# Optimization experiments

Hardware: AMD Instinct MI355X
Metric: run time of the kernel (lower is better)

The kernel has to match this reference:

```python
import jax, jax.numpy as jnp
import numpy as np

B, S, D, H, NI, NB = 512, 200, 256, 4, 100000, 2
DH = D // H
NEG = float(-(2**32) + 1)
SCALE = float(1.0 / np.sqrt(DH))


def ln(x, g, b, eps=1e-3):
    # keras LayerNormalization (default epsilon=1e-3)
    m = jnp.mean(x, axis=-1, keepdims=True)
    v = jnp.var(x, axis=-1, keepdims=True)
    return (x - m) * jax.lax.rsqrt(v + eps) * g + b


def setup_inputs() -> dict:
    key = jax.random.key(0)
    ks = jax.random.split(key, 10)
    s = 0.02
    return {
        "input_ids": jax.random.randint(ks[0], (B, S), 0, NI + 1, dtype=jnp.int32),
        "item_emb": jax.random.normal(ks[1], (NI + 1, D), jnp.float32) * s,
        "pos_emb": jax.random.normal(ks[2], (S, D), jnp.float32) * s,
        "ln1_g": jnp.ones((NB, D), jnp.float32),
        "ln1_b": jnp.zeros((NB, D), jnp.float32),
        "wq": jax.random.normal(ks[3], (NB, D, D), jnp.float32) * s,
        "bq": jnp.zeros((NB, D), jnp.float32),
        "wk": jax.random.normal(ks[4], (NB, D, D), jnp.float32) * s,
        "bk": jnp.zeros((NB, D), jnp.float32),
        "wv": jax.random.normal(ks[5], (NB, D, D), jnp.float32) * s,
        "bv": jnp.zeros((NB, D), jnp.float32),
        "ln2_g": jnp.ones((NB, D), jnp.float32),
        "ln2_b": jnp.zeros((NB, D), jnp.float32),
        "wd": jax.random.normal(ks[6], (NB, D, D), jnp.float32) * s,
        "bd": jnp.zeros((NB, D), jnp.float32),
        "seq_g": jnp.ones((D,), jnp.float32),
        "seq_b": jnp.zeros((D,), jnp.float32),
        "out_item_emb": jax.random.normal(ks[7], (NI, D), jnp.float32) * s,
    }


def reference(input_ids, item_emb, pos_emb, ln1_g, ln1_b, wq, bq, wk, bk, wv, bv,
              ln2_g, ln2_b, wd, bd, seq_g, seq_b, out_item_emb):
    seq = item_emb[input_ids] + pos_emb[None]                      # [B,S,D]
    mask = (input_ids != NI).astype(seq.dtype)[:, :, None]        # pad id == num_items
    causal = jnp.tril(jnp.ones((S, S), bool))
    for i in range(NB):
        x = ln(seq, ln1_g[i], ln1_b[i])                            # queries (pre-norm)
        q = (x @ wq[i] + bq[i]).reshape(B, S, H, DH).transpose(0, 2, 1, 3)
        k = (seq @ wk[i] + bk[i]).reshape(B, S, H, DH).transpose(0, 2, 1, 3)
        v = (seq @ wv[i] + bv[i]).reshape(B, S, H, DH).transpose(0, 2, 1, 3)
        scores = jnp.einsum('bhqd,bhkd->bhqk', q, k) * SCALE       # [B,H,S,S]
        scores = jnp.where(causal, scores, NEG)
        attn = jax.nn.softmax(scores, axis=-1)
        o = jnp.einsum('bhqk,bhkd->bhqd', attn, v)
        o = o.transpose(0, 2, 1, 3).reshape(B, S, D)
        x2 = o + x                                                 # residual to normed queries
        y = jax.nn.relu(ln(x2, ln2_g[i], ln2_b[i]) @ wd[i] + bd[i])
        seq = (y + x2) * mask
    seq_emb = ln(seq[:, -1, :], seq_g, seq_b)                      # [B,D]
    return seq_emb @ out_item_emb.T                                # [B,num_items], linear act
```

## Files before the change

kernel.cpp:

```cpp
#include <hip/hip_runtime.h>
#include <hip/hip_bf16.h>
#include <cstdint>
#include <cstddef>

namespace {
constexpr int B = 512, S = 200, D = 256, H = 4, DH = 64, NI = 100000;
constexpr float EPS = 1e-3f;
constexpr float SCALE = 0.125f;
}

typedef __attribute__((ext_vector_type(8))) short bf16x8;
typedef __attribute__((ext_vector_type(4))) float f32x4;

__device__ inline unsigned short f2b(float f) {
  union { float f; unsigned int u; } v; v.f = f;
  unsigned int r = v.u + 0x7FFFu + ((v.u >> 16) & 1u);
  return (unsigned short)(r >> 16);
}

__device__ inline float b2f(unsigned short u) {
  union { unsigned int i; float f; } x; x.i = (unsigned int)u << 16; return x.f;
}

__device__ inline bf16x8 pack8(float4 a, float4 b) {
  bf16x8 r;
  r[0] = (short)f2b(a.x); r[1] = (short)f2b(a.y); r[2] = (short)f2b(a.z); r[3] = (short)f2b(a.w);
  r[4] = (short)f2b(b.x); r[5] = (short)f2b(b.y); r[6] = (short)f2b(b.z); r[7] = (short)f2b(b.w);
  return r;
}

__device__ inline ushort4 pack4(float4 a) {
  ushort4 r;
  r.x = f2b(a.x); r.y = f2b(a.y); r.z = f2b(a.z); r.w = f2b(a.w);
  return r;
}

__device__ inline float4 unpack4(ushort4 u) {
  float4 r; r.x = b2f(u.x); r.y = b2f(u.y); r.z = b2f(u.z); r.w = b2f(u.w); return r;
}

__device__ inline void gload_lds16(const unsigned short* g, unsigned short* l) {
  __builtin_amdgcn_global_load_lds((const __attribute__((address_space(1))) void*)g,
                                   (__attribute__((address_space(3))) void*)l, 16, 0, 0);
}

__global__ void cvt_wout_k(const float* __restrict__ src, unsigned short* __restrict__ dst) {
  const int total = NI * D / 8;
  for (int i = blockIdx.x * blockDim.x + threadIdx.x; i < total; i += gridDim.x * blockDim.x) {
    const float4 a = *(const float4*)(src + (size_t)i * 8);
    const float4 b = *(const float4*)(src + (size_t)i * 8 + 4);
    *(bf16x8*)(dst + (size_t)i * 8) = pack8(a, b);
  }
}

__global__ void cvt_wt_k(const float* __restrict__ wq, const float* __restrict__ wk,
                         const float* __restrict__ wv, const float* __restrict__ wd,
                         unsigned short* __restrict__ dst) {
  const int t = blockIdx.x * 256 + threadIdx.x;
  const int w = t >> 14, rem = t & 16383;
  const int k = rem >> 6, n4 = (rem & 63) * 4;
  const int blk = w >> 2, which = w & 3;
  const float* src = (which == 0 ? wq : which == 1 ? wk : which == 2 ? wv : wd) + blk * 65536;
  const float4 v = *(const float4*)(src + k * 256 + n4);
  unsigned short* d = dst + w * 65536;
  d[(n4 + 0) * 256 + k] = f2b(v.x);
  d[(n4 + 1) * 256 + k] = f2b(v.y);
  d[(n4 + 2) * 256 + k] = f2b(v.z);
  d[(n4 + 3) * 256 + k] = f2b(v.w);
}

__global__ void embed_k(const int* __restrict__ ids, const float* __restrict__ ie,
                        const float* __restrict__ pe, unsigned short* __restrict__ seq_bf) {
  const int total = B * S * (D / 4);
  for (int i = blockIdx.x * blockDim.x + threadIdx.x; i < total; i += gridDim.x * blockDim.x) {
    const int bs = i >> 6;
    const int d4 = (i & 63) << 2;
    const int id = ids[bs];
    const int s = bs % S;
    float4 a = *(const float4*)(ie + (size_t)id * D + d4);
    const float4 p = *(const float4*)(pe + (size_t)s * D + d4);
    a.x += p.x; a.y += p.y; a.z += p.z; a.w += p.w;
    *(ushort4*)(seq_bf + (size_t)bs * D + d4) = pack4(a);
  }
}

__global__ __launch_bounds__(256) void ln_bf_k(const unsigned short* __restrict__ in,
                                               size_t in_stride,
                                               const float* __restrict__ g, const float* __restrict__ b,
                                               unsigned short* __restrict__ outp, int nrows) {
  const int row = blockIdx.x * 4 + (threadIdx.x >> 6);
  if (row >= nrows) return;
  const int lane = threadIdx.x & 63;
  const float4 v = unpack4(*(const ushort4*)(in + (size_t)row * in_stride + (lane << 2)));
  float s = v.x + v.y + v.z + v.w;
  float ss = v.x * v.x + v.y * v.y + v.z * v.z + v.w * v.w;
#pragma unroll
  for (int off = 32; off; off >>= 1) {
    s += __shfl_xor(s, off);
    ss += __shfl_xor(ss, off);
  }
  const float mean = s * (1.f / D);
  const float rs = rsqrtf(ss * (1.f / D) - mean * mean + EPS);
  const float4 gv = *(const float4*)(g + (lane << 2));
  const float4 bv = *(const float4*)(b + (lane << 2));
  float4 o;
  o.x = (v.x - mean) * rs * gv.x + bv.x;
  o.y = (v.y - mean) * rs * gv.y + bv.y;
  o.z = (v.z - mean) * rs * gv.z + bv.z;
  o.w = (v.w - mean) * rs * gv.w + bv.w;
  *(ushort4*)(outp + (size_t)row * D + (lane << 2)) = pack4(o);
}

__global__ __launch_bounds__(256) void ln2x2_k(const unsigned short* __restrict__ x_bf,
                                               const unsigned short* __restrict__ o_bf,
                                               const float* __restrict__ g2, const float* __restrict__ b2,
                                               float* __restrict__ x2_out,
                                               unsigned short* __restrict__ t_bf, int nrows) {
  const int row = blockIdx.x * 4 + (threadIdx.x >> 6);
  if (row >= nrows) return;
  const int lane = threadIdx.x & 63;
  const float4 xv = unpack4(*(const ushort4*)(x_bf + (size_t)row * D + (lane << 2)));
  const float4 ov = unpack4(*(const ushort4*)(o_bf + (size_t)row * D + (lane << 2)));
  float4 x2;
  x2.x = xv.x + ov.x; x2.y = xv.y + ov.y; x2.z = xv.z + ov.z; x2.w = xv.w + ov.w;
  *(float4*)(x2_out + (size_t)row * D + (lane << 2)) = x2;
  float s2 = x2.x + x2.y + x2.z + x2.w;
  float ss2 = x2.x * x2.x + x2.y * x2.y + x2.z * x2.z + x2.w * x2.w;
#pragma unroll
  for (int off = 32; off; off >>= 1) {
    s2 += __shfl_xor(s2, off);
    ss2 += __shfl_xor(ss2, off);
  }
  const float mean2 = s2 * (1.f / D);
  const float rs2 = rsqrtf(ss2 * (1.f / D) - mean2 * mean2 + EPS);
  const float4 g2v = *(const float4*)(g2 + (lane << 2));
  const float4 b2v = *(const float4*)(b2 + (lane << 2));
  float4 t;
  t.x = (x2.x - mean2) * rs2 * g2v.x + b2v.x;
  t.y = (x2.y - mean2) * rs2 * g2v.y + b2v.y;
  t.z = (x2.z - mean2) * rs2 * g2v.z + b2v.z;
  t.w = (x2.w - mean2) * rs2 * g2v.w + b2v.w;
  *(ushort4*)(t_bf + (size_t)row * D + (lane << 2)) = pack4(t);
}

template <int RELU, int UPD>
__global__ __launch_bounds__(512) void bgemm2_k(const unsigned short* __restrict__ A,
                                                const unsigned short* __restrict__ Wt,
                                                const float* __restrict__ bias,
                                                unsigned short* __restrict__ Cbf,
                                                const float* __restrict__ x2,
                                                const int* __restrict__ ids) {
  __shared__ unsigned short As[128 * 64];
  __shared__ unsigned short Bs[256 * 64];
  const int tid = threadIdx.x, w = tid >> 6, lane = tid & 63;
  const int kb = lane >> 4, ln = lane & 15;
  const int m0 = blockIdx.x * 128;
  const int wm = w & 1, wn = w >> 1;

  f32x4 acc[4][4];
#pragma unroll
  for (int i = 0; i < 4; ++i)
#pragma unroll
    for (int j = 0; j < 4; ++j) acc[i][j] = (f32x4){0.f, 0.f, 0.f, 0.f};

  for (int ks = 0; ks < 4; ++ks) {
    const int ko = ks * 64;
#pragma unroll
    for (int r = 0; r < 2; ++r) {
      const int g = (w * 2 + r) * 64 + lane;
      const int row = g >> 3, gc = g & 7;
      gload_lds16(A + (size_t)(m0 + row) * 256 + ko + ((gc ^ (row & 7)) << 3),
                  As + (size_t)(w * 2 + r) * 512);
    }
#pragma unroll
    for (int r = 0; r < 4; ++r) {
      const int g = (w * 4 + r) * 64 + lane;
      const int row = g >> 3, gc = g & 7;
      gload_lds16(Wt + (size_t)row * 256 + ko + ((gc ^ (row & 7)) << 3),
                  Bs + (size_t)(w * 4 + r) * 512);
    }
    __syncthreads();
#pragma unroll
    for (int h = 0; h < 2; ++h) {
      bf16x8 af[4], bfr[4];
#pragma unroll
      for (int i = 0; i < 4; ++i) {
        const int ar = wm * 64 + i * 16 + ln;
        af[i] = *(const bf16x8*)(As + ar * 64 + (((h * 64 + kb * 16) ^ ((ar & 7) << 4)) >> 1));
        const int br = wn * 64 + i * 16 + ln;
        bfr[i] = *(const bf16x8*)(Bs + br * 64 + (((h * 64 + kb * 16) ^ ((br & 7) << 4)) >> 1));
      }
#pragma unroll
      for (int i = 0; i < 4; ++i)
#pragma unroll
        for (int j = 0; j < 4; ++j)
          acc[i][j] = __builtin_amdgcn_mfma_f32_16x16x32_bf16(af[i], bfr[j], acc[i][j], 0, 0, 0);
    }
    __syncthreads();
  }

  const int crow0 = m0 + wm * 64 + kb * 4;
  const int ccol0 = wn * 64 + ln;
  float mk[4][4];
  if (UPD) {
#pragma unroll
    for (int i = 0; i < 4; ++i)
#pragma unroll
      for (int r = 0; r < 4; ++r) mk[i][r] = (ids[crow0 + i * 16 + r] != NI) ? 1.f : 0.f;
  }
#pragma unroll
  for (int j = 0; j < 4; ++j) {
    const int col = ccol0 + j * 16;
    const float bj = bias[col];
#pragma unroll
    for (int i = 0; i < 4; ++i) {
#pragma unroll
      for (int r = 0; r < 4; ++r) {
        const int row = crow0 + i * 16 + r;
        float v = acc[i][j][r] + bj;
        if (RELU) v = fmaxf(v, 0.f);
        if (UPD) v = (v + x2[(size_t)row * 256 + col]) * mk[i][r];
        Cbf[(size_t)row * 256 + col] = f2b(v);
      }
    }
  }
}

template <int NSWAP, int GUARD>
__global__ __launch_bounds__(256) void bgemm_k(const unsigned short* __restrict__ A,
                                               const unsigned short* __restrict__ Wt,
                                               float* __restrict__ C, int M, int N) {
  __shared__ unsigned short As[128 * 64];
  __shared__ unsigned short Bs[128 * 64];
  const int tid = threadIdx.x, w = tid >> 6, lane = tid & 63;
  const int kb = lane >> 4, ln = lane & 15;
  const int m0 = (NSWAP ? blockIdx.x : blockIdx.y) * 128;
  const int n0 = (NSWAP ? blockIdx.y : blockIdx.x) * 128;
  const int wm = w & 1, wn = w >> 1;
  const int rl = lane >> 3;
  const int cb = (lane & 7) << 4;

  f32x4 acc[4][4];
#pragma unroll
  for (int i = 0; i < 4; ++i)
#pragma unroll
    for (int j = 0; j < 4; ++j) acc[i][j] = (f32x4){0.f, 0.f, 0.f, 0.f};

  for (int ks = 0; ks < 4; ++ks) {
    const int ko = ks * 64;
#pragma unroll
    for (int c = 0; c < 4; ++c) {
      const int arow = w * 32 + c * 8 + rl;
      const int sw = (arow & 7) << 4;
      const int cu = (cb ^ sw) >> 1;
      gload_lds16(A + (size_t)(m0 + arow) * 256 + ko + cu, As + (w * 32 + c * 8) * 64);
      int br = n0 + arow;
      if (GUARD && br > N - 1) br = N - 1;
      gload_lds16(Wt + (size_t)br * 256 + ko + cu, Bs + (w * 32 + c * 8) * 64);
    }
    __syncthreads();
#pragma unroll
    for (int h = 0; h < 2; ++h) {
      bf16x8 af[4], bfr[4];
#pragma unroll
      for (int i = 0; i < 4; ++i) {
        const int ar = wm * 64 + i * 16 + ln;
        af[i] = *(const bf16x8*)(As + ar * 64 + (((h * 64 + kb * 16) ^ ((ar & 7) << 4)) >> 1));
        const int br = wn * 64 + i * 16 + ln;
        bfr[i] = *(const bf16x8*)(Bs + br * 64 + (((h * 64 + kb * 16) ^ ((br & 7) << 4)) >> 1));
      }
#pragma unroll
      for (int i = 0; i < 4; ++i)
#pragma unroll
        for (int j = 0; j < 4; ++j)
          acc[i][j] = __builtin_amdgcn_mfma_f32_16x16x32_bf16(af[i], bfr[j], acc[i][j], 0, 0, 0);
    }
    __syncthreads();
  }

  const int crow0 = m0 + wm * 64 + kb * 4;
  const int ccol0 = n0 + wn * 64 + ln;
#pragma unroll
  for (int j = 0; j < 4; ++j) {
    const int col = ccol0 + j * 16;
    if (GUARD && col >= N) continue;
#pragma unroll
    for (int i = 0; i < 4; ++i) {
#pragma unroll
      for (int r = 0; r < 4; ++r) {
        const int row = crow0 + i * 16 + r;
        C[(size_t)row * N + col] = acc[i][j][r];
      }
    }
  }
}

__global__ __launch_bounds__(256) void attn2_k(const unsigned short* __restrict__ Q,
                                               const unsigned short* __restrict__ Kg,
                                               const unsigned short* __restrict__ Vg,
                                               unsigned short* __restrict__ O) {
  __shared__ unsigned short Ks[13312];
  __shared__ unsigned short Vt[13312];
  __shared__ unsigned short Ps[4 * 3328];
  const int b = blockIdx.x >> 2;
  const int h = blockIdx.x & 3;
  const int tid = threadIdx.x, w = tid >> 6, lane = tid & 63;
  const int kb = lane >> 4, ln = lane & 15;
  const size_t base = (size_t)b * S * D + h * DH;

  for (int s = w; s < 26; s += 4) {
    const int t = s >> 1, h2 = s & 1;
    int krow = t * 16 + ln; if (krow > S - 1) krow = S - 1;
    gload_lds16(Kg + base + (size_t)krow * D + h2 * 32 + kb * 8, Ks + s * 512);
  }
  for (int g = tid; g < 200 * 8; g += 256) {
    const int key = g >> 3, d0 = (g & 7) * 8;
    const bf16x8 v = *(const bf16x8*)(Vg + base + (size_t)key * D + d0);
#pragma unroll
    for (int i = 0; i < 8; ++i) {
      const int d = d0 + i, ct = d >> 4, cl = d & 15;
      int addr;
      if (key < 192) addr = (((ct * 6 + (key >> 5)) * 4 + ((key >> 3) & 3)) * 16 + cl) * 8 + (key & 7);
      else           addr = 12288 + ((ct * 2 + ((key >> 3) & 1)) * 16 + cl) * 8 + (key & 7);
      Vt[addr] = (unsigned short)v[i];
    }
  }
  if (tid < 64) {
    const int ct = tid >> 4, cl = tid & 15;
    *(bf16x8*)(Vt + 12288 + ((ct * 2 + 1) * 16 + cl) * 8) = (bf16x8)0;
  }
  __syncthreads();
  unsigned short* Pw = Ps + w * 3328;

  for (int q0 = w * 16; q0 < S; q0 += 64) {
    int qr = q0 + ln; if (qr > S - 1) qr = S - 1;
    const unsigned short* qp = Q + base + (size_t)qr * D + kb * 8;
    const bf16x8 aq0 = *(const bf16x8*)(qp);
    const bf16x8 aq1 = *(const bf16x8*)(qp + 32);
    f32x4 sc[13];
#pragma unroll
    for (int t = 0; t < 13; ++t) {
      f32x4 a = {0.f, 0.f, 0.f, 0.f};
      a = __builtin_amdgcn_mfma_f32_16x16x32_bf16(aq0, *(const bf16x8*)(Ks + (t * 2 + 0) * 512 + lane * 8), a, 0, 0, 0);
      a = __builtin_amdgcn_mfma_f32_16x16x32_bf16(aq1, *(const bf16x8*)(Ks + (t * 2 + 1) * 512 + lane * 8), a, 0, 0, 0);
      sc[t] = a;
    }
    float inv[4];
#pragma unroll
    for (int r = 0; r < 4; ++r) {
      const int q = q0 + kb * 4 + r;
      const int qrow = kb * 4 + r;
      float m = -1e30f;
#pragma unroll
      for (int t = 0; t < 13; ++t) {
        const int j = t * 16 + ln;
        float s = sc[t][r] * SCALE;
        s = (j <= q) ? s : -1e30f;
        sc[t][r] = s;
        m = fmaxf(m, s);
      }
      m = fmaxf(m, __shfl_xor(m, 1));
      m = fmaxf(m, __shfl_xor(m, 2));
      m = fmaxf(m, __shfl_xor(m, 4));
      m = fmaxf(m, __shfl_xor(m, 8));
      float sm = 0.f;
#pragma unroll
      for (int t = 0; t < 13; ++t) {
        const float e = __expf(sc[t][r] - m);
        sm += e;
        int addr;
        if (t < 12) addr = (((t >> 1) * 4 + ((2 * t + (ln >> 3)) & 3)) * 16 + qrow) * 8 + (ln & 7);
        else        addr = 3072 + ((ln >> 3) * 16 + qrow) * 8 + (ln & 7);
        Pw[addr] = f2b(e);
      }
      sm += __shfl_xor(sm, 1);
      sm += __shfl_xor(sm, 2);
      sm += __shfl_xor(sm, 4);
      sm += __shfl_xor(sm, 8);
      inv[r] = 1.f / sm;
    }
#pragma unroll
    for (int ct = 0; ct < 4; ++ct) {
      f32x4 a = {0.f, 0.f, 0.f, 0.f};
#pragma unroll
      for (int kt = 0; kt < 6; ++kt) {
        const bf16x8 pa = *(const bf16x8*)(Pw + ((kt * 4 + kb) * 16 + ln) * 8);
        const bf16x8 vb = *(const bf16x8*)(Vt + (((ct * 6 + kt) * 4 + kb) * 16 + ln) * 8);
        a = __builtin_amdgcn_mfma_f32_16x16x32_bf16(pa, vb, a, 0, 0, 0);
      }
      {
        bf16x8 pa = (bf16x8)0, vb = (bf16x8)0;
        if (kb < 2) {
          pa = *(const bf16x8*)(Pw + 3072 + (kb * 16 + ln) * 8);
          vb = *(const bf16x8*)(Vt + 12288 + ((ct * 2 + kb) * 16 + ln) * 8);
        }
        a = __builtin_amdgcn_mfma_f32_16x16x32_bf16(pa, vb, a, 0, 0, 0);
      }
#pragma unroll
      for (int r = 0; r < 4; ++r) {
        const int q = q0 + kb * 4 + r;
        if (q < S) O[base + (size_t)q * D + ct * 16 + ln] = f2b(a[r] * inv[r]);
      }
    }
  }
}

extern "C" void kernel_launch(void* const* d_in, const int* in_sizes, int n_in,
                              void* d_out, int out_size, void* d_ws, size_t ws_size,
                              hipStream_t stream) {
  const int* ids        = (const int*)d_in[0];
  const float* item_emb = (const float*)d_in[1];
  const float* pos_emb  = (const float*)d_in[2];
  const float* ln1_g    = (const float*)d_in[3];
  const float* ln1_b    = (const float*)d_in[4];
  const float* wq       = (const float*)d_in[5];
  const float* bq       = (const float*)d_in[6];
  const float* wk       = (const float*)d_in[7];
  const float* bk       = (const float*)d_in[8];
  const float* wv       = (const float*)d_in[9];
  const float* bv       = (const float*)d_in[10];
  const float* ln2_g    = (const float*)d_in[11];
  const float* ln2_b    = (const float*)d_in[12];
  const float* wd       = (const float*)d_in[13];
  const float* bd       = (const float*)d_in[14];
  const float* seq_g    = (const float*)d_in[15];
  const float* seq_b    = (const float*)d_in[16];
  const float* w_out    = (const float*)d_in[17];
  float* out = (float*)d_out;

  char* wsb = (char*)d_ws;
  unsigned short* o_bf   = (unsigned short*)(wsb + 0);
  float* x2              = (float*)(wsb + 104857600);
  unsigned short* seq_bf = (unsigned short*)(wsb + 209715200);
  unsigned short* x_bf   = (unsigned short*)(wsb + 262144000);
  unsigned short* q_bf   = (unsigned short*)(wsb + 314572800);
  unsigned short* k_bf   = (unsigned short*)(wsb + 367001600);
  unsigned short* v_bf   = (unsigned short*)(wsb + 419430400);
  unsigned short* wob    = (unsigned short*)(wsb + 471859200);
  unsigned short* wtb    = (unsigned short*)(wsb + 523059200);
  unsigned short* semb   = (unsigned short*)(wsb + 524107776);

  const int M = B * S;
  const int ln_grid = (M + 3) / 4;

  cvt_wout_k<<<2048, 256, 0, stream>>>(w_out, wob);
  cvt_wt_k<<<512, 256, 0, stream>>>(wq, wk, wv, wd, wtb);
  embed_k<<<2048, 256, 0, stream>>>(ids, item_emb, pos_emb, seq_bf);

  for (int blk = 0; blk < 2; ++blk) {
    const float* l1g = ln1_g + blk * D;
    const float* l1b = ln1_b + blk * D;
    const float* l2g = ln2_g + blk * D;
    const float* l2b = ln2_b + blk * D;
    const unsigned short* WT = wtb + (size_t)blk * 4 * 65536;

    bgemm2_k<0, 0><<<800, 512, 0, stream>>>(seq_bf, WT + 1 * 65536, bk + blk * D, k_bf, nullptr, nullptr);
    bgemm2_k<0, 0><<<800, 512, 0, stream>>>(seq_bf, WT + 2 * 65536, bv + blk * D, v_bf, nullptr, nullptr);
    ln_bf_k<<<ln_grid, 256, 0, stream>>>(seq_bf, D, l1g, l1b, x_bf, M);
    bgemm2_k<0, 0><<<800, 512, 0, stream>>>(x_bf, WT + 0 * 65536, bq + blk * D, q_bf, nullptr, nullptr);
    attn2_k<<<B * H, 256, 0, stream>>>(q_bf, k_bf, v_bf, o_bf);
    ln2x2_k<<<ln_grid, 256, 0, stream>>>(x_bf, o_bf, l2g, l2b, x2, x_bf, M);
    bgemm2_k<1, 1><<<800, 512, 0, stream>>>(x_bf, WT + 3 * 65536, bd + blk * D, seq_bf, x2, ids);
  }

  ln_bf_k<<<(B + 3) / 4, 256, 0, stream>>>(seq_bf + (size_t)(S - 1) * D, (size_t)S * D,
                                           seq_g, seq_b, semb, B);
  bgemm_k<1, 1><<<dim3(4, 782), 256, 0, stream>>>(semb, wob, out, B, NI);
}
```

Before: 841.5 us.

## Fuse output-weight conversion into final GEMM, restructure attention with register softmax

```diff
diff --git a/kernel.cpp b/kernel.cpp
--- a/kernel.cpp
+++ b/kernel.cpp
@@ -39,18 +39,15 @@
   float4 r; r.x = b2f(u.x); r.y = b2f(u.y); r.z = b2f(u.z); r.w = b2f(u.w); return r;
 }
 
+__device__ inline unsigned cvtpk(float lo, float hi) {
+  unsigned r;
+  asm("v_cvt_pk_bf16_f32 %0, %1, %2" : "=v"(r) : "v"(lo), "v"(hi));
+  return r;
+}
+
 __device__ inline void gload_lds16(const unsigned short* g, unsigned short* l) {
   __builtin_amdgcn_global_load_lds((const __attribute__((address_space(1))) void*)g,
                                    (__attribute__((address_space(3))) void*)l, 16, 0, 0);
-}
-
-__global__ void cvt_wout_k(const float* __restrict__ src, unsigned short* __restrict__ dst) {
-  const int total = NI * D / 8;
-  for (int i = blockIdx.x * blockDim.x + threadIdx.x; i < total; i += gridDim.x * blockDim.x) {
-    const float4 a = *(const float4*)(src + (size_t)i * 8);
-    const float4 b = *(const float4*)(src + (size_t)i * 8 + 4);
-    *(bf16x8*)(dst + (size_t)i * 8) = pack8(a, b);
-  }
 }
 
 __global__ void cvt_wt_k(const float* __restrict__ wq, const float* __restrict__ wk,
@@ -114,7 +111,7 @@
 __global__ __launch_bounds__(256) void ln2x2_k(const unsigned short* __restrict__ x_bf,
                                                const unsigned short* __restrict__ o_bf,
                                                const float* __restrict__ g2, const float* __restrict__ b2,
-                                               float* __restrict__ x2_out,
+                                               unsigned short* __restrict__ x2b,
                                                unsigned short* __restrict__ t_bf, int nrows) {
   const int row = blockIdx.x * 4 + (threadIdx.x >> 6);
   if (row >= nrows) return;
@@ -123,7 +120,7 @@
   const float4 ov = unpack4(*(const ushort4*)(o_bf + (size_t)row * D + (lane << 2)));
   float4 x2;
   x2.x = xv.x + ov.x; x2.y = xv.y + ov.y; x2.z = xv.z + ov.z; x2.w = xv.w + ov.w;
-  *(float4*)(x2_out + (size_t)row * D + (lane << 2)) = x2;
+  *(ushort4*)(x2b + (size_t)row * D + (lane << 2)) = pack4(x2);
   float s2 = x2.x + x2.y + x2.z + x2.w;
   float ss2 = x2.x * x2.x + x2.y * x2.y + x2.z * x2.z + x2.w * x2.w;
 #pragma unroll
@@ -148,8 +145,8 @@
                                                 const unsigned short* __restrict__ Wt,
                                                 const float* __restrict__ bias,
                                                 unsigned short* __restrict__ Cbf,
-                                                const float* __restrict__ x2,
-                                                const int* __restrict__ ids) {
+                                                const unsigned short* __restrict__ x2b,
+                                                const int* __restrict__ ids, float osc) {
   __shared__ unsigned short As[128 * 64];
   __shared__ unsigned short Bs[256 * 64];
   const int tid = threadIdx.x, w = tid >> 6, lane = tid & 63;
@@ -217,25 +214,24 @@
 #pragma unroll
       for (int r = 0; r < 4; ++r) {
         const int row = crow0 + i * 16 + r;
-        float v = acc[i][j][r] + bj;
+        float v = (acc[i][j][r] + bj) * osc;
         if (RELU) v = fmaxf(v, 0.f);
-        if (UPD) v = (v + x2[(size_t)row * 256 + col]) * mk[i][r];
+        if (UPD) v = (v + b2f(x2b[(size_t)row * 256 + col])) * mk[i][r];
         Cbf[(size_t)row * 256 + col] = f2b(v);
       }
     }
   }
 }
 
-template <int NSWAP, int GUARD>
-__global__ __launch_bounds__(256) void bgemm_k(const unsigned short* __restrict__ A,
-                                               const unsigned short* __restrict__ Wt,
-                                               float* __restrict__ C, int M, int N) {
+__global__ __launch_bounds__(256) void bgemm3_k(const unsigned short* __restrict__ A,
+                                                const float* __restrict__ Wf,
+                                                float* __restrict__ C, int M, int N) {
   __shared__ unsigned short As[128 * 64];
   __shared__ unsigned short Bs[128 * 64];
   const int tid = threadIdx.x, w = tid >> 6, lane = tid & 63;
   const int kb = lane >> 4, ln = lane & 15;
-  const int m0 = (NSWAP ? blockIdx.x : blockIdx.y) * 128;
-  const int n0 = (NSWAP ? blockIdx.y : blockIdx.x) * 128;
+  const int m0 = blockIdx.x * 128;
+  const int n0 = blockIdx.y * 128;
   const int wm = w & 1, wn = w >> 1;
   const int rl = lane >> 3;
   const int cb = (lane & 7) << 4;
@@ -254,9 +250,16 @@
       const int sw = (arow & 7) << 4;
       const int cu = (cb ^ sw) >> 1;
       gload_lds16(A + (size_t)(m0 + arow) * 256 + ko + cu, As + (w * 32 + c * 8) * 64);
-      int br = n0 + arow;
-      if (GUARD && br > N - 1) br = N - 1;
-      gload_lds16(Wt + (size_t)br * 256 + ko + cu, Bs + (w * 32 + c * 8) * 64);
+    }
+#pragma unroll
+    for (int c = 0; c < 4; ++c) {
+      const int g = c * 256 + tid;
+      const int row = g >> 3, gcs = g & 7;
+      int br = n0 + row; if (br > N - 1) br = N - 1;
+      const float* src = Wf + (size_t)br * 256 + ko + gcs * 8;
+      const float4 f0 = *(const float4*)src;
+      const float4 f1 = *(const float4*)(src + 4);
+      *(bf16x8*)(Bs + row * 64 + ((gcs ^ (row & 7)) << 3)) = pack8(f0, f1);
     }
     __syncthreads();
 #pragma unroll
@@ -283,7 +286,7 @@
 #pragma unroll
   for (int j = 0; j < 4; ++j) {
     const int col = ccol0 + j * 16;
-    if (GUARD && col >= N) continue;
+    if (col >= N) continue;
 #pragma unroll
     for (int i = 0; i < 4; ++i) {
 #pragma unroll
@@ -295,111 +298,129 @@
   }
 }
 
-__global__ __launch_bounds__(256) void attn2_k(const unsigned short* __restrict__ Q,
-                                               const unsigned short* __restrict__ Kg,
-                                               const unsigned short* __restrict__ Vg,
-                                               unsigned short* __restrict__ O) {
+__global__ __launch_bounds__(256) void vT_k(const unsigned short* __restrict__ V,
+                                            unsigned short* __restrict__ VT) {
+  __shared__ unsigned short tile[64][72];
+  const int bh = blockIdx.x >> 2;
+  const int sc = blockIdx.x & 3;
+  const int b = bh >> 2, h = bh & 3;
+  const int k0 = sc * 64;
+  const int tid = threadIdx.x;
+  for (int g = tid; g < 512; g += 256) {
+    const int kr = g >> 3, dq = g & 7;
+    bf16x8 v = (bf16x8)0;
+    const int key = k0 + kr;
+    if (key < 200) v = *(const bf16x8*)(V + (size_t)(b * 200 + key) * 256 + h * 64 + dq * 8);
+    *(bf16x8*)(&tile[kr][dq * 8]) = v;
+  }
+  __syncthreads();
+  for (int g = tid; g < 512; g += 256) {
+    const int d = g & 63, kgl = g >> 6;
+    const int kg = (k0 >> 3) + kgl;
+    if (kg >= 26) continue;
+    bf16x8 o;
+#pragma unroll
+    for (int j = 0; j < 8; ++j) o[j] = tile[kgl * 8 + j][d];
+    *(bf16x8*)(VT + (size_t)bh * 13312 + ((size_t)kg * 64 + d) * 8) = o;
+  }
+}
+
+__global__ __launch_bounds__(256, 3) void attn3_k(const unsigned short* __restrict__ Q,
+                                                  const unsigned short* __restrict__ Kg,
+                                                  const unsigned short* __restrict__ VT,
+                                                  unsigned short* __restrict__ O) {
   __shared__ unsigned short Ks[13312];
-  __shared__ unsigned short Vt[13312];
-  __shared__ unsigned short Ps[4 * 3328];
+  __shared__ unsigned short Vs[13312];
   const int b = blockIdx.x >> 2;
   const int h = blockIdx.x & 3;
   const int tid = threadIdx.x, w = tid >> 6, lane = tid & 63;
   const int kb = lane >> 4, ln = lane & 15;
   const size_t base = (size_t)b * S * D + h * DH;
+  const unsigned short* vt = VT + (size_t)(b * 4 + h) * 13312;
 
   for (int s = w; s < 26; s += 4) {
     const int t = s >> 1, h2 = s & 1;
     int krow = t * 16 + ln; if (krow > S - 1) krow = S - 1;
     gload_lds16(Kg + base + (size_t)krow * D + h2 * 32 + kb * 8, Ks + s * 512);
-  }
-  for (int g = tid; g < 200 * 8; g += 256) {
-    const int key = g >> 3, d0 = (g & 7) * 8;
-    const bf16x8 v = *(const bf16x8*)(Vg + base + (size_t)key * D + d0);
-#pragma unroll
-    for (int i = 0; i < 8; ++i) {
-      const int d = d0 + i, ct = d >> 4, cl = d & 15;
-      int addr;
-      if (key < 192) addr = (((ct * 6 + (key >> 5)) * 4 + ((key >> 3) & 3)) * 16 + cl) * 8 + (key & 7);
-      else           addr = 12288 + ((ct * 2 + ((key >> 3) & 1)) * 16 + cl) * 8 + (key & 7);
-      Vt[addr] = (unsigned short)v[i];
-    }
-  }
-  if (tid < 64) {
-    const int ct = tid >> 4, cl = tid & 15;
-    *(bf16x8*)(Vt + 12288 + ((ct * 2 + 1) * 16 + cl) * 8) = (bf16x8)0;
+    gload_lds16(vt + s * 512 + lane * 8, Vs + s * 512);
   }
   __syncthreads();
-  unsigned short* Pw = Ps + w * 3328;
 
   for (int q0 = w * 16; q0 < S; q0 += 64) {
     int qr = q0 + ln; if (qr > S - 1) qr = S - 1;
     const unsigned short* qp = Q + base + (size_t)qr * D + kb * 8;
-    const bf16x8 aq0 = *(const bf16x8*)(qp);
-    const bf16x8 aq1 = *(const bf16x8*)(qp + 32);
+    const bf16x8 bq0 = *(const bf16x8*)(qp);
+    const bf16x8 bq1 = *(const bf16x8*)(qp + 32);
     f32x4 sc[13];
 #pragma unroll
     for (int t = 0; t < 13; ++t) {
       f32x4 a = {0.f, 0.f, 0.f, 0.f};
-      a = __builtin_amdgcn_mfma_f32_16x16x32_bf16(aq0, *(const bf16x8*)(Ks + (t * 2 + 0) * 512 + lane * 8), a, 0, 0, 0);
-      a = __builtin_amdgcn_mfma_f32_16x16x32_bf16(aq1, *(const bf16x8*)(Ks + (t * 2 + 1) * 512 + lane * 8), a, 0, 0, 0);
+      a = __builtin_amdgcn_mfma_f32_16x16x32_bf16(*(const bf16x8*)(Ks + (t * 2 + 0) * 512 + lane * 8), bq0, a, 0, 0, 0);
+      a = __builtin_amdgcn_mfma_f32_16x16x32_bf16(*(const bf16x8*)(Ks + (t * 2 + 1) * 512 + lane * 8), bq1, a, 0, 0, 0);
       sc[t] = a;
     }
-    float inv[4];
-#pragma unroll
-    for (int r = 0; r < 4; ++r) {
-      const int q = q0 + kb * 4 + r;
-      const int qrow = kb * 4 + r;
-      float m = -1e30f;
-#pragma unroll
-      for (int t = 0; t < 13; ++t) {
-        const int j = t * 16 + ln;
-        float s = sc[t][r] * SCALE;
-        s = (j <= q) ? s : -1e30f;
+    const int q = q0 + ln;
+    float m = -1e30f;
+#pragma unroll
+    for (int t = 0; t < 13; ++t) {
+#pragma unroll
+      for (int r = 0; r < 4; ++r) {
+        const int key = t * 16 + kb * 4 + r;
+        float s = sc[t][r];
+        s = (key <= q) ? s : -1e30f;
         sc[t][r] = s;
         m = fmaxf(m, s);
       }
-      m = fmaxf(m, __shfl_xor(m, 1));
-      m = fmaxf(m, __shfl_xor(m, 2));
-      m = fmaxf(m, __shfl_xor(m, 4));
-      m = fmaxf(m, __shfl_xor(m, 8));
-      float sm = 0.f;
-#pragma unroll
-      for (int t = 0; t < 13; ++t) {
+    }
+    m = fmaxf(m, __shfl_xor(m, 16));
+    m = fmaxf(m, __shfl_xor(m, 32));
+    float sm = 0.f;
+#pragma unroll
+    for (int t = 0; t < 13; ++t) {
+#pragma unroll
+      for (int r = 0; r < 4; ++r) {
         const float e = __expf(sc[t][r] - m);
+        sc[t][r] = e;
         sm += e;
-        int addr;
-        if (t < 12) addr = (((t >> 1) * 4 + ((2 * t + (ln >> 3)) & 3)) * 16 + qrow) * 8 + (ln & 7);
-        else        addr = 3072 + ((ln >> 3) * 16 + qrow) * 8 + (ln & 7);
-        Pw[addr] = f2b(e);
-      }
-      sm += __shfl_xor(sm, 1);
-      sm += __shfl_xor(sm, 2);
-      sm += __shfl_xor(sm, 4);
-      sm += __shfl_xor(sm, 8);
-      inv[r] = 1.f / sm;
+      }
+    }
+    sm += __shfl_xor(sm, 16);
+    sm += __shfl_xor(sm, 32);
+    const float inv = 1.f / sm;
+    int4 pg[7];
+#pragma unroll
+    for (int i = 0; i < 7; ++i) pg[i] = (int4){0, 0, 0, 0};
+    const int s0 = ((kb & 1) << 5) + ln;
+#pragma unroll
+    for (int t = 0; t < 13; ++t) {
+      const int lo = (int)cvtpk(sc[t][0] * inv, sc[t][1] * inv);
+      const int hi = (int)cvtpk(sc[t][2] * inv, sc[t][3] * inv);
+      const int b0 = __shfl(lo, s0);
+      const int b1 = __shfl(hi, s0);
+      const int b2 = __shfl(lo, s0 + 16);
+      const int b3 = __shfl(hi, s0 + 16);
+      if ((t & 1) == (kb >> 1)) pg[t >> 1] = (int4){b0, b1, b2, b3};
     }
 #pragma unroll
     for (int ct = 0; ct < 4; ++ct) {
       f32x4 a = {0.f, 0.f, 0.f, 0.f};
 #pragma unroll
       for (int kt = 0; kt < 6; ++kt) {
-        const bf16x8 pa = *(const bf16x8*)(Pw + ((kt * 4 + kb) * 16 + ln) * 8);
-        const bf16x8 vb = *(const bf16x8*)(Vt + (((ct * 6 + kt) * 4 + kb) * 16 + ln) * 8);
+        const bf16x8 pa = *(const bf16x8*)&pg[kt];
+        const bf16x8 vb = *(const bf16x8*)(Vs + ((kt * 4 + kb) * 64 + ct * 16 + ln) * 8);
         a = __builtin_amdgcn_mfma_f32_16x16x32_bf16(pa, vb, a, 0, 0, 0);
       }
       {
-        bf16x8 pa = (bf16x8)0, vb = (bf16x8)0;
-        if (kb < 2) {
-          pa = *(const bf16x8*)(Pw + 3072 + (kb * 16 + ln) * 8);
-          vb = *(const bf16x8*)(Vt + 12288 + ((ct * 2 + kb) * 16 + ln) * 8);
-        }
+        const int kg6 = 24 + (kb & 1);
+        const bf16x8 vb = *(const bf16x8*)(Vs + (kg6 * 64 + ct * 16 + ln) * 8);
+        bf16x8 pa = (bf16x8)0;
+        if (kb < 2) pa = *(const bf16x8*)&pg[6];
         a = __builtin_amdgcn_mfma_f32_16x16x32_bf16(pa, vb, a, 0, 0, 0);
       }
 #pragma unroll
       for (int r = 0; r < 4; ++r) {
-        const int q = q0 + kb * 4 + r;
-        if (q < S) O[base + (size_t)q * D + ct * 16 + ln] = f2b(a[r] * inv[r]);
+        const int qq = q0 + kb * 4 + r;
+        if (qq < S) O[base + (size_t)qq * D + ct * 16 + ln] = f2b(a[r]);
       }
     }
   }
@@ -429,21 +450,20 @@
   float* out = (float*)d_out;
 
   char* wsb = (char*)d_ws;
-  unsigned short* o_bf   = (unsigned short*)(wsb + 0);
-  float* x2              = (float*)(wsb + 104857600);
-  unsigned short* seq_bf = (unsigned short*)(wsb + 209715200);
-  unsigned short* x_bf   = (unsigned short*)(wsb + 262144000);
-  unsigned short* q_bf   = (unsigned short*)(wsb + 314572800);
-  unsigned short* k_bf   = (unsigned short*)(wsb + 367001600);
-  unsigned short* v_bf   = (unsigned short*)(wsb + 419430400);
-  unsigned short* wob    = (unsigned short*)(wsb + 471859200);
-  unsigned short* wtb    = (unsigned short*)(wsb + 523059200);
-  unsigned short* semb   = (unsigned short*)(wsb + 524107776);
+  unsigned short* seq_bf = (unsigned short*)(wsb + 0);
+  unsigned short* x_bf   = (unsigned short*)(wsb + 52428800);
+  unsigned short* q_bf   = (unsigned short*)(wsb + 104857600);
+  unsigned short* k_bf   = (unsigned short*)(wsb + 157286400);
+  unsigned short* v_bf   = (unsigned short*)(wsb + 209715200);
+  unsigned short* o_bf   = (unsigned short*)(wsb + 262144000);
+  unsigned short* x2b    = (unsigned short*)(wsb + 314572800);
+  unsigned short* vt     = (unsigned short*)(wsb + 367001600);
+  unsigned short* wtb    = (unsigned short*)(wsb + 421527552);
+  unsigned short* semb   = (unsigned short*)(wsb + 422576128);
 
   const int M = B * S;
   const int ln_grid = (M + 3) / 4;
 
-  cvt_wout_k<<<2048, 256, 0, stream>>>(w_out, wob);
   cvt_wt_k<<<512, 256, 0, stream>>>(wq, wk, wv, wd, wtb);
   embed_k<<<2048, 256, 0, stream>>>(ids, item_emb, pos_emb, seq_bf);
 
@@ -454,16 +474,17 @@
     const float* l2b = ln2_b + blk * D;
     const unsigned short* WT = wtb + (size_t)blk * 4 * 65536;
 
-    bgemm2_k<0, 0><<<800, 512, 0, stream>>>(seq_bf, WT + 1 * 65536, bk + blk * D, k_bf, nullptr, nullptr);
-    bgemm2_k<0, 0><<<800, 512, 0, stream>>>(seq_bf, WT + 2 * 65536, bv + blk * D, v_bf, nullptr, nullptr);
+    bgemm2_k<0, 0><<<800, 512, 0, stream>>>(seq_bf, WT + 1 * 65536, bk + blk * D, k_bf, nullptr, nullptr, 1.f);
+    bgemm2_k<0, 0><<<800, 512, 0, stream>>>(seq_bf, WT + 2 * 65536, bv + blk * D, v_bf, nullptr, nullptr, 1.f);
+    vT_k<<<B * H * 4, 256, 0, stream>>>(v_bf, vt);
     ln_bf_k<<<ln_grid, 256, 0, stream>>>(seq_bf, D, l1g, l1b, x_bf, M);
-    bgemm2_k<0, 0><<<800, 512, 0, stream>>>(x_bf, WT + 0 * 65536, bq + blk * D, q_bf, nullptr, nullptr);
-    attn2_k<<<B * H, 256, 0, stream>>>(q_bf, k_bf, v_bf, o_bf);
-    ln2x2_k<<<ln_grid, 256, 0, stream>>>(x_bf, o_bf, l2g, l2b, x2, x_bf, M);
-    bgemm2_k<1, 1><<<800, 512, 0, stream>>>(x_bf, WT + 3 * 65536, bd + blk * D, seq_bf, x2, ids);
+    bgemm2_k<0, 0><<<800, 512, 0, stream>>>(x_bf, WT + 0 * 65536, bq + blk * D, q_bf, nullptr, nullptr, SCALE);
+    attn3_k<<<B * H, 256, 0, stream>>>(q_bf, k_bf, vt, o_bf);
+    ln2x2_k<<<ln_grid, 256, 0, stream>>>(x_bf, o_bf, l2g, l2b, x2b, x_bf, M);
+    bgemm2_k<1, 1><<<800, 512, 0, stream>>>(x_bf, WT + 3 * 65536, bd + blk * D, seq_bf, x2b, ids, 1.f);
   }
 
   ln_bf_k<<<(B + 3) / 4, 256, 0, stream>>>(seq_bf + (size_t)(S - 1) * D, (size_t)S * D,
                                            seq_g, seq_b, semb, B);
-  bgemm_k<1, 1><<<dim3(4, 782), 256, 0, stream>>>(semb, wob, out, B, NI);
-}
+  bgemm3_k<<<dim3(4, 782), 256, 0, stream>>>(semb, w_out, out, B, NI);
+}
```

Result: slower. 862.6 us (+2.5%).

## Fuse embed with LN1, LN1 into dense epilogue, fold scale, convert Wout on the fly

Applied to the files above, without the earlier changes.

```diff
diff --git a/kernel.cpp b/kernel.cpp
--- a/kernel.cpp
+++ b/kernel.cpp
@@ -42,15 +42,6 @@
 __device__ inline void gload_lds16(const unsigned short* g, unsigned short* l) {
   __builtin_amdgcn_global_load_lds((const __attribute__((address_space(1))) void*)g,
                                    (__attribute__((address_space(3))) void*)l, 16, 0, 0);
-}
-
-__global__ void cvt_wout_k(const float* __restrict__ src, unsigned short* __restrict__ dst) {
-  const int total = NI * D / 8;
-  for (int i = blockIdx.x * blockDim.x + threadIdx.x; i < total; i += gridDim.x * blockDim.x) {
-    const float4 a = *(const float4*)(src + (size_t)i * 8);
-    const float4 b = *(const float4*)(src + (size_t)i * 8 + 4);
-    *(bf16x8*)(dst + (size_t)i * 8) = pack8(a, b);
-  }
 }
 
 __global__ void cvt_wt_k(const float* __restrict__ wq, const float* __restrict__ wk,
@@ -69,19 +60,39 @@
   d[(n4 + 3) * 256 + k] = f2b(v.w);
 }
 
-__global__ void embed_k(const int* __restrict__ ids, const float* __restrict__ ie,
-                        const float* __restrict__ pe, unsigned short* __restrict__ seq_bf) {
-  const int total = B * S * (D / 4);
-  for (int i = blockIdx.x * blockDim.x + threadIdx.x; i < total; i += gridDim.x * blockDim.x) {
-    const int bs = i >> 6;
-    const int d4 = (i & 63) << 2;
-    const int id = ids[bs];
-    const int s = bs % S;
-    float4 a = *(const float4*)(ie + (size_t)id * D + d4);
-    const float4 p = *(const float4*)(pe + (size_t)s * D + d4);
-    a.x += p.x; a.y += p.y; a.z += p.z; a.w += p.w;
-    *(ushort4*)(seq_bf + (size_t)bs * D + d4) = pack4(a);
-  }
+__global__ __launch_bounds__(256) void embed_ln_k(const int* __restrict__ ids,
+                                                  const float* __restrict__ ie,
+                                                  const float* __restrict__ pe,
+                                                  const float* __restrict__ g1,
+                                                  const float* __restrict__ b1,
+                                                  unsigned short* __restrict__ seq_bf,
+                                                  unsigned short* __restrict__ x_bf) {
+  const int row = blockIdx.x * 4 + (threadIdx.x >> 6);
+  const int lane = threadIdx.x & 63;
+  const int id = ids[row];
+  const int s = row % S;
+  float4 v = *(const float4*)(ie + (size_t)id * D + (lane << 2));
+  const float4 p = *(const float4*)(pe + (size_t)s * D + (lane << 2));
+  v.x += p.x; v.y += p.y; v.z += p.z; v.w += p.w;
+  *(ushort4*)(seq_bf + (size_t)row * D + (lane << 2)) = pack4(v);
+  const float4 vb = unpack4(pack4(v));
+  float su = vb.x + vb.y + vb.z + vb.w;
+  float ss = vb.x * vb.x + vb.y * vb.y + vb.z * vb.z + vb.w * vb.w;
+#pragma unroll
+  for (int off = 32; off; off >>= 1) {
+    su += __shfl_xor(su, off);
+    ss += __shfl_xor(ss, off);
+  }
+  const float mean = su * (1.f / D);
+  const float rs = rsqrtf(ss * (1.f / D) - mean * mean + EPS);
+  const float4 gv = *(const float4*)(g1 + (lane << 2));
+  const float4 bv = *(const float4*)(b1 + (lane << 2));
+  float4 o;
+  o.x = (vb.x - mean) * rs * gv.x + bv.x;
+  o.y = (vb.y - mean) * rs * gv.y + bv.y;
+  o.z = (vb.z - mean) * rs * gv.z + bv.z;
+  o.w = (vb.w - mean) * rs * gv.w + bv.w;
+  *(ushort4*)(x_bf + (size_t)row * D + (lane << 2)) = pack4(o);
 }
 
 __global__ __launch_bounds__(256) void ln_bf_k(const unsigned short* __restrict__ in,
@@ -114,7 +125,7 @@
 __global__ __launch_bounds__(256) void ln2x2_k(const unsigned short* __restrict__ x_bf,
                                                const unsigned short* __restrict__ o_bf,
                                                const float* __restrict__ g2, const float* __restrict__ b2,
-                                               float* __restrict__ x2_out,
+                                               unsigned short* __restrict__ x2b,
                                                unsigned short* __restrict__ t_bf, int nrows) {
   const int row = blockIdx.x * 4 + (threadIdx.x >> 6);
   if (row >= nrows) return;
@@ -123,7 +134,7 @@
   const float4 ov = unpack4(*(const ushort4*)(o_bf + (size_t)row * D + (lane << 2)));
   float4 x2;
   x2.x = xv.x + ov.x; x2.y = xv.y + ov.y; x2.z = xv.z + ov.z; x2.w = xv.w + ov.w;
-  *(float4*)(x2_out + (size_t)row * D + (lane << 2)) = x2;
+  *(ushort4*)(x2b + (size_t)row * D + (lane << 2)) = pack4(x2);
   float s2 = x2.x + x2.y + x2.z + x2.w;
   float ss2 = x2.x * x2.x + x2.y * x2.y + x2.z * x2.z + x2.w * x2.w;
 #pragma unroll
@@ -143,13 +154,16 @@
   *(ushort4*)(t_bf + (size_t)row * D + (lane << 2)) = pack4(t);
 }
 
-template <int RELU, int UPD>
+template <int RELU, int UPD, int LN1>
 __global__ __launch_bounds__(512) void bgemm2_k(const unsigned short* __restrict__ A,
                                                 const unsigned short* __restrict__ Wt,
                                                 const float* __restrict__ bias,
                                                 unsigned short* __restrict__ Cbf,
-                                                const float* __restrict__ x2,
-                                                const int* __restrict__ ids) {
+                                                const unsigned short* __restrict__ x2b,
+                                                const int* __restrict__ ids, float osc,
+                                                const float* __restrict__ g1,
+                                                const float* __restrict__ b1,
+                                                unsigned short* __restrict__ x1) {
   __shared__ unsigned short As[128 * 64];
   __shared__ unsigned short Bs[256 * 64];
   const int tid = threadIdx.x, w = tid >> 6, lane = tid & 63;
@@ -217,25 +231,82 @@
 #pragma unroll
       for (int r = 0; r < 4; ++r) {
         const int row = crow0 + i * 16 + r;
-        float v = acc[i][j][r] + bj;
+        float v = (acc[i][j][r] + bj) * osc;
         if (RELU) v = fmaxf(v, 0.f);
-        if (UPD) v = (v + x2[(size_t)row * 256 + col]) * mk[i][r];
-        Cbf[(size_t)row * 256 + col] = f2b(v);
-      }
-    }
-  }
-}
-
-template <int NSWAP, int GUARD>
-__global__ __launch_bounds__(256) void bgemm_k(const unsigned short* __restrict__ A,
-                                               const unsigned short* __restrict__ Wt,
-                                               float* __restrict__ C, int M, int N) {
+        if (UPD) v = (v + b2f(x2b[(size_t)row * 256 + col])) * mk[i][r];
+        const unsigned short vb = f2b(v);
+        Cbf[(size_t)row * 256 + col] = vb;
+        if (LN1) acc[i][j][r] = b2f(vb);
+      }
+    }
+  }
+
+  if (LN1) {
+    float s_[4][4], ss_[4][4];
+#pragma unroll
+    for (int i = 0; i < 4; ++i)
+#pragma unroll
+      for (int r = 0; r < 4; ++r) {
+        float s = 0.f, ss = 0.f;
+#pragma unroll
+        for (int j = 0; j < 4; ++j) { const float v = acc[i][j][r]; s += v; ss += v * v; }
+#pragma unroll
+        for (int off = 1; off < 16; off <<= 1) {
+          s += __shfl_xor(s, off);
+          ss += __shfl_xor(ss, off);
+        }
+        s_[i][r] = s; ss_[i][r] = ss;
+      }
+    float* red = (float*)As;
+    if (ln == 0) {
+#pragma unroll
+      for (int i = 0; i < 4; ++i)
+#pragma unroll
+        for (int r = 0; r < 4; ++r) {
+          const int rl = wm * 64 + kb * 4 + i * 16 + r;
+          red[rl * 8 + wn * 2 + 0] = s_[i][r];
+          red[rl * 8 + wn * 2 + 1] = ss_[i][r];
+        }
+    }
+    __syncthreads();
+#pragma unroll
+    for (int i = 0; i < 4; ++i)
+#pragma unroll
+      for (int r = 0; r < 4; ++r) {
+        const int rl = wm * 64 + kb * 4 + i * 16 + r;
+        float S = 0.f, SS = 0.f;
+#pragma unroll
+        for (int q = 0; q < 4; ++q) { S += red[rl * 8 + q * 2]; SS += red[rl * 8 + q * 2 + 1]; }
+        const float mean = S * (1.f / D);
+        s_[i][r] = mean;
+        ss_[i][r] = rsqrtf(SS * (1.f / D) - mean * mean + EPS);
+      }
+#pragma unroll
+    for (int j = 0; j < 4; ++j) {
+      const int col = ccol0 + j * 16;
+      const float gc = g1[col], bc = b1[col];
+#pragma unroll
+      for (int i = 0; i < 4; ++i) {
+#pragma unroll
+        for (int r = 0; r < 4; ++r) {
+          const int row = crow0 + i * 16 + r;
+          const float xv = (acc[i][j][r] - s_[i][r]) * ss_[i][r] * gc + bc;
+          x1[(size_t)row * 256 + col] = f2b(xv);
+        }
+      }
+    }
+  }
+}
+
+__global__ __launch_bounds__(256) void bgemm3_k(const unsigned short* __restrict__ A,
+                                                const float* __restrict__ Wf,
+                                                float* __restrict__ C, int M, int N) {
   __shared__ unsigned short As[128 * 64];
   __shared__ unsigned short Bs[128 * 64];
   const int tid = threadIdx.x, w = tid >> 6, lane = tid & 63;
   const int kb = lane >> 4, ln = lane & 15;
-  const int m0 = (NSWAP ? blockIdx.x : blockIdx.y) * 128;
-  const int n0 = (NSWAP ? blockIdx.y : blockIdx.x) * 128;
+  const int m0 = blockIdx.x * 128;
+  const int n0 = blockIdx.y * 128;
   const int wm = w & 1, wn = w >> 1;
   const int rl = lane >> 3;
   const int cb = (lane & 7) << 4;
@@ -254,9 +325,16 @@
       const int sw = (arow & 7) << 4;
       const int cu = (cb ^ sw) >> 1;
       gload_lds16(A + (size_t)(m0 + arow) * 256 + ko + cu, As + (w * 32 + c * 8) * 64);
-      int br = n0 + arow;
-      if (GUARD && br > N - 1) br = N - 1;
-      gload_lds16(Wt + (size_t)br * 256 + ko + cu, Bs + (w * 32 + c * 8) * 64);
+    }
+#pragma unroll
+    for (int c = 0; c < 4; ++c) {
+      const int g = c * 256 + tid;
+      const int row = g >> 3, gcs = g & 7;
+      int br = n0 + row; if (br > N - 1) br = N - 1;
+      const float* src = Wf + (size_t)br * 256 + ko + gcs * 8;
+      const float4 f0 = *(const float4*)src;
+      const float4 f1 = *(const float4*)(src + 4);
+      *(bf16x8*)(Bs + row * 64 + ((gcs ^ (row & 7)) << 3)) = pack8(f0, f1);
     }
     __syncthreads();
 #pragma unroll
@@ -283,7 +361,7 @@
 #pragma unroll
   for (int j = 0; j < 4; ++j) {
     const int col = ccol0 + j * 16;
-    if (GUARD && col >= N) continue;
+    if (col >= N) continue;
 #pragma unroll
     for (int i = 0; i < 4; ++i) {
 #pragma unroll
@@ -295,10 +373,10 @@
   }
 }
 
-__global__ __launch_bounds__(256) void attn2_k(const unsigned short* __restrict__ Q,
-                                               const unsigned short* __restrict__ Kg,
-                                               const unsigned short* __restrict__ Vg,
-                                               unsigned short* __restrict__ O) {
+__global__ __launch_bounds__(256) void attn_k(const unsigned short* __restrict__ Q,
+                                              const unsigned short* __restrict__ Kg,
+                                              const unsigned short* __restrict__ Vg,
+                                              unsigned short* __restrict__ O) {
   __shared__ unsigned short Ks[13312];
   __shared__ unsigned short Vt[13312];
   __shared__ unsigned short Ps[4 * 3328];
@@ -354,7 +432,7 @@
 #pragma unroll
       for (int t = 0; t < 13; ++t) {
         const int j = t * 16 + ln;
-        float s = sc[t][r] * SCALE;
+        float s = sc[t][r];
         s = (j <= q) ? s : -1e30f;
         sc[t][r] = s;
         m = fmaxf(m, s);
@@ -429,41 +507,45 @@
   float* out = (float*)d_out;
 
   char* wsb = (char*)d_ws;
-  unsigned short* o_bf   = (unsigned short*)(wsb + 0);
-  float* x2              = (float*)(wsb + 104857600);
-  unsigned short* seq_bf = (unsigned short*)(wsb + 209715200);
-  unsigned short* x_bf   = (unsigned short*)(wsb + 262144000);
-  unsigned short* q_bf   = (unsigned short*)(wsb + 314572800);
-  unsigned short* k_bf   = (unsigned short*)(wsb + 367001600);
-  unsigned short* v_bf   = (unsigned short*)(wsb + 419430400);
-  unsigned short* wob    = (unsigned short*)(wsb + 471859200);
-  unsigned short* wtb    = (unsigned short*)(wsb + 523059200);
-  unsigned short* semb   = (unsigned short*)(wsb + 524107776);
+  unsigned short* seq_bf = (unsigned short*)(wsb + 0);
+  unsigned short* x_bf   = (unsigned short*)(wsb + 52428800);
+  unsigned short* q_bf   = (unsigned short*)(wsb + 104857600);
+  unsigned short* k_bf   = (unsigned short*)(wsb + 157286400);
+  unsigned short* v_bf   = (unsigned short*)(wsb + 209715200);
+  unsigned short* o_bf   = (unsigned short*)(wsb + 262144000);
+  unsigned short* x2b    = (unsigned short*)(wsb + 314572800);
+  unsigned short* wtb    = (unsigned short*)(wsb + 367001600);
+  unsigned short* semb   = (unsigned short*)(wsb + 368050176);
 
   const int M = B * S;
   const int ln_grid = (M + 3) / 4;
 
-  cvt_wout_k<<<2048, 256, 0, stream>>>(w_out, wob);
   cvt_wt_k<<<512, 256, 0, stream>>>(wq, wk, wv, wd, wtb);
-  embed_k<<<2048, 256, 0, stream>>>(ids, item_emb, pos_emb, seq_bf);
+  embed_ln_k<<<ln_grid, 256, 0, stream>>>(ids, item_emb, pos_emb, ln1_g, ln1_b, seq_bf, x_bf);
 
   for (int blk = 0; blk < 2; ++blk) {
-    const float* l1g = ln1_g + blk * D;
-    const float* l1b = ln1_b + blk * D;
     const float* l2g = ln2_g + blk * D;
     const float* l2b = ln2_b + blk * D;
     const unsigned short* WT = wtb + (size_t)blk * 4 * 65536;
 
-    bgemm2_k<0, 0><<<800, 512, 0, stream>>>(seq_bf, WT + 1 * 65536, bk + blk * D, k_bf, nullptr, nullptr);
-    bgemm2_k<0, 0><<<800, 512, 0, stream>>>(seq_bf, WT + 2 * 65536, bv + blk * D, v_bf, nullptr, nullptr);
-    ln_bf_k<<<ln_grid, 256, 0, stream>>>(seq_bf, D, l1g, l1b, x_bf, M);
-    bgemm2_k<0, 0><<<800, 512, 0, stream>>>(x_bf, WT + 0 * 65536, bq + blk * D, q_bf, nullptr, nullptr);
-    attn2_k<<<B * H, 256, 0, stream>>>(q_bf, k_bf, v_bf, o_bf);
-    ln2x2_k<<<ln_grid, 256, 0, stream>>>(x_bf, o_bf, l2g, l2b, x2, x_bf, M);
-    bgemm2_k<1, 1><<<800, 512, 0, stream>>>(x_bf, WT + 3 * 65536, bd + blk * D, seq_bf, x2, ids);
+    bgemm2_k<0, 0, 0><<<800, 512, 0, stream>>>(seq_bf, WT + 1 * 65536, bk + blk * D, k_bf,
+                                               nullptr, nullptr, 1.f, nullptr, nullptr, nullptr);
+    bgemm2_k<0, 0, 0><<<800, 512, 0, stream>>>(seq_bf, WT + 2 * 65536, bv + blk * D, v_bf,
+                                               nullptr, nullptr, 1.f, nullptr, nullptr, nullptr);
+    bgemm2_k<0, 0, 0><<<800, 512, 0, stream>>>(x_bf, WT + 0 * 65536, bq + blk * D, q_bf,
+                                               nullptr, nullptr, SCALE, nullptr, nullptr, nullptr);
+    attn_k<<<B * H, 256, 0, stream>>>(q_bf, k_bf, v_bf, o_bf);
+    ln2x2_k<<<ln_grid, 256, 0, stream>>>(x_bf, o_bf, l2g, l2b, x2b, q_bf, M);
+    if (blk == 0) {
+      bgemm2_k<1, 1, 1><<<800, 512, 0, stream>>>(q_bf, WT + 3 * 65536, bd + blk * D, seq_bf,
+                                                 x2b, ids, 1.f, ln1_g + D, ln1_b + D, x_bf);
+    } else {
+      bgemm2_k<1, 1, 0><<<800, 512, 0, stream>>>(q_bf, WT + 3 * 65536, bd + blk * D, seq_bf,
+                                                 x2b, ids, 1.f, nullptr, nullptr, nullptr);
+    }
   }
 
   ln_bf_k<<<(B + 3) / 4, 256, 0, stream>>>(seq_bf + (size_t)(S - 1) * D, (size_t)S * D,
                                            seq_g, seq_b, semb, B);
-  bgemm_k<1, 1><<<dim3(4, 782), 256, 0, stream>>>(semb, wob, out, B, NI);
-}
+  bgemm3_k<<<dim3(4, 782), 256, 0, stream>>>(semb, w_out, out, B, NI);
+}
```

New measurement: 775.9 us. -7.8%, faster.
